# Optimization experiments

Hardware: AMD Instinct MI355X
Metric: run time of the kernel (lower is better)

Reference implementation:

```python
import math
import jax, jax.numpy as jnp
import numpy as np

T, B, F = 2048, 8, 768
N_HEAD = 12            # only used for the scale, per original code
N_CHUNK = 3            # chunk(3, -1) -> 3 effective heads
SCALE = math.sqrt(F // N_HEAD)  # sqrt(64) = 8.0


def setup_inputs() -> dict:
    key = jax.random.key(0)
    ks = jax.random.split(key, 9)
    s = 1.0 / math.sqrt(F)
    return {
        "x": jax.random.normal(ks[0], (T, B, F), jnp.float32),
        "Wq": jax.random.normal(ks[1], (F, F), jnp.float32) * s,
        "bq": jax.random.normal(ks[2], (F,), jnp.float32) * s,
        "Wk": jax.random.normal(ks[3], (F, F), jnp.float32) * s,
        "bk": jax.random.normal(ks[4], (F,), jnp.float32) * s,
        "Wv": jax.random.normal(ks[5], (F, F), jnp.float32) * s,
        "bv": jax.random.normal(ks[6], (F,), jnp.float32) * s,
        "Wo": jax.random.normal(ks[7], (F, F), jnp.float32) * s,
        "bo": jax.random.normal(ks[8], (F,), jnp.float32) * s,
    }


def reference(x, Wq, bq, Wk, bk, Wv, bv, Wo, bo):
    # x: (T, B, F). Linear is y = x @ W.T + b (torch convention).
    t, b, f = x.shape
    dh = f // N_CHUNK
    scale = jnp.asarray(SCALE, x.dtype)
    # project then split into 3 chunks along feature dim -> (T, B, 3, dh)
    q = (x @ Wq.T + bq).reshape(t, b, N_CHUNK, dh)
    k = (x @ Wk.T + bk).reshape(t, b, N_CHUNK, dh)
    v = (x @ Wv.T + bv).reshape(t, b, N_CHUNK, dh)
    # scores: (B, H, T, T)
    scores = jnp.einsum('tbhd,sbhd->bhts', q, k) / scale
    attn = jax.nn.softmax(scores, axis=-1)
    # output: (T, B, H, dh) -> (T, B, F)
    o = jnp.einsum('bhts,sbhd->tbhd', attn, v).reshape(t, b, f)
    return o @ Wo.T + bo
```

## Files before the change

kernel.cpp:

```cpp
#include <hip/hip_runtime.h>
#include <cstdint>
#include <cstddef>

#define T_SEQ 2048
#define B_SZ  8
#define F_DIM 768
#define H_CNT 3
#define DH    256

typedef float floatx4 __attribute__((ext_vector_type(4)));
typedef short bf16x8  __attribute__((ext_vector_type(8)));

static __device__ __forceinline__ unsigned short f2bf(float f) {
    union { float f; unsigned int i; } x; x.f = f;
    unsigned int r = (x.i + 0x7fffu + ((x.i >> 16) & 1u)) >> 16;
    return (unsigned short)r;
}

static __device__ __forceinline__ bf16x8 load8f(const float* __restrict__ p) {
    const floatx4 a = *(const floatx4*)p;
    const floatx4 b = *(const floatx4*)(p + 4);
    bf16x8 r;
#pragma unroll
    for (int i = 0; i < 4; ++i) r[i] = (short)f2bf(a[i]);
#pragma unroll
    for (int i = 0; i < 4; ++i) r[i + 4] = (short)f2bf(b[i]);
    return r;
}

#define ASYNC16(g, l) __builtin_amdgcn_global_load_lds( \
    (__attribute__((address_space(1))) void*)(void*)(g), \
    (__attribute__((address_space(3))) void*)(l), 16, 0, 0)

template<int AMODE, int CMODE>
__global__ __launch_bounds__(256, 2) void gemm_nt(
    const void* __restrict__ Av,
    const float* __restrict__ W,
    const float* __restrict__ bias,
    void* __restrict__ Cv,
    int M, int N, int K, float scale)
{
    __shared__ __align__(16) unsigned short As[128 * 32];
    __shared__ __align__(16) unsigned short Bs[128 * 32];

    const int tid  = threadIdx.x;
    const int wave = tid >> 6;
    const int lane = tid & 63;
    const int m0 = blockIdx.y * 128;
    const int n0 = blockIdx.x * 128;
    const int wm = (wave >> 1) * 64;
    const int wn = (wave & 1) * 64;
    const int q4 = lane >> 4;
    const int rr = lane & 15;

    const int lrow = lane >> 2;
    const int lk8  = (lane & 3) * 8;
    const int ar0 = wave * 16 + lrow;
    const int ar1 = (wave + 4) * 16 + lrow;

    floatx4 acc[4][4];
#pragma unroll
    for (int i = 0; i < 4; ++i)
#pragma unroll
        for (int j = 0; j < 4; ++j) acc[i][j] = (floatx4)0.0f;

    for (int k0 = 0; k0 < K; k0 += 32) {
        bf16x8 a0, a1;
        if (AMODE == 0) {
            const float* A = (const float*)Av;
            a0 = load8f(A + (size_t)(m0 + ar0) * K + k0 + lk8);
            a1 = load8f(A + (size_t)(m0 + ar1) * K + k0 + lk8);
        } else {
            const unsigned short* A = (const unsigned short*)Av;
            a0 = *(const bf16x8*)(A + (size_t)(m0 + ar0) * K + k0 + lk8);
            a1 = *(const bf16x8*)(A + (size_t)(m0 + ar1) * K + k0 + lk8);
        }
        bf16x8 b0 = load8f(W + (size_t)(n0 + ar0) * K + k0 + lk8);
        bf16x8 b1 = load8f(W + (size_t)(n0 + ar1) * K + k0 + lk8);
        __syncthreads();
        *(bf16x8*)&As[ar0 * 32 + lk8] = a0;
        *(bf16x8*)&As[ar1 * 32 + lk8] = a1;
        *(bf16x8*)&Bs[ar0 * 32 + lk8] = b0;
        *(bf16x8*)&Bs[ar1 * 32 + lk8] = b1;
        __syncthreads();

        bf16x8 af[4], bfv[4];
#pragma unroll
        for (int mt = 0; mt < 4; ++mt)
            af[mt] = *(const bf16x8*)&As[(wm + mt * 16 + rr) * 32 + q4 * 8];
#pragma unroll
        for (int nt = 0; nt < 4; ++nt)
            bfv[nt] = *(const bf16x8*)&Bs[(wn + nt * 16 + rr) * 32 + q4 * 8];
#pragma unroll
        for (int mt = 0; mt < 4; ++mt)
#pragma unroll
            for (int nt = 0; nt < 4; ++nt)
                acc[mt][nt] = __builtin_amdgcn_mfma_f32_16x16x32_bf16(af[mt], bfv[nt], acc[mt][nt], 0, 0, 0);
    }

#pragma unroll
    for (int nt = 0; nt < 4; ++nt) {
        const int col = n0 + wn + nt * 16 + rr;
        const float bv = bias[col];
#pragma unroll
        for (int mt = 0; mt < 4; ++mt) {
#pragma unroll
            for (int r = 0; r < 4; ++r) {
                const int row = m0 + wm + mt * 16 + q4 * 4 + r;
                const float v = (acc[mt][nt][r] + bv) * scale;
                if (CMODE == 2) {
                    ((float*)Cv)[(size_t)row * N + col] = v;
                } else {
                    const int t = row >> 3, bb = row & 7;
                    const int h = col >> 8, d = col & 255;
                    const size_t hb = (size_t)(bb * H_CNT + h) * (T_SEQ * DH);
                    size_t idx;
                    if (CMODE == 3) {
                        const int sblk = t >> 4, rrq = t & 15;
                        const int kc = d >> 5, q4v = (d >> 3) & 3, e = d & 7;
                        idx = hb + (size_t)(((sblk * 8 + kc) * 64 + q4v * 16 + rrq) * 8 + e);
                    } else {
                        const int skc = t >> 5, q4v = (t >> 3) & 3, e = t & 7;
                        const int dblk = d >> 4, rrq = d & 15;
                        idx = hb + (size_t)(((skc * 16 + dblk) * 64 + q4v * 16 + rrq) * 8 + e);
                    }
                    ((unsigned short*)Cv)[idx] = f2bf(v);
                }
            }
        }
    }
}

__global__ __launch_bounds__(256, 3) void attn_kernel(
    const unsigned short* __restrict__ Qf,
    const unsigned short* __restrict__ Kf,
    const unsigned short* __restrict__ Vf,
    unsigned short* __restrict__ Ob)
{
    __shared__ __align__(16) unsigned short Ks[8192];
    __shared__ __align__(16) unsigned short Vs[8192];
    __shared__ __align__(16) unsigned short Plds[4][512];

    const int tid  = threadIdx.x;
    const int wave = tid >> 6;
    const int lane = tid & 63;
    const int q4 = lane >> 4;
    const int rr = lane & 15;
    const int bh = blockIdx.y;
    const int b  = bh / H_CNT;
    const int h  = bh % H_CNT;
    const size_t hb = (size_t)bh * (T_SEQ * DH);

    const int qblk = blockIdx.x * 4 + wave;
    bf16x8 qf[8];
#pragma unroll
    for (int kc = 0; kc < 8; ++kc)
        qf[kc] = *(const bf16x8*)(Qf + hb + ((size_t)(qblk * 8 + kc) * 64 + lane) * 8);

    float m_[4], l_[4];
#pragma unroll
    for (int r = 0; r < 4; ++r) { m_[r] = -1e9f; l_[r] = 0.0f; }
    floatx4 oacc[16];
#pragma unroll
    for (int nt = 0; nt < 16; ++nt) oacc[nt] = (floatx4)0.0f;

    const int so = wave * 512 + lane * 8;

    for (int s0 = 0; s0 < T_SEQ; s0 += 32) {
        const unsigned short* kg = Kf + hb + (size_t)(s0 >> 4) * 4096;
        const unsigned short* vg = Vf + hb + (size_t)(s0 >> 5) * 8192;
#pragma unroll
        for (int rnd = 0; rnd < 4; ++rnd) {
            ASYNC16(kg + rnd * 2048 + so, (unsigned short*)Ks + rnd * 2048 + wave * 512);
            ASYNC16(vg + rnd * 2048 + so, (unsigned short*)Vs + rnd * 2048 + wave * 512);
        }
        __syncthreads();

        floatx4 sacc[2] = { (floatx4)0.0f, (floatx4)0.0f };
#pragma unroll
        for (int nt = 0; nt < 2; ++nt)
#pragma unroll
            for (int kc = 0; kc < 8; ++kc) {
                bf16x8 kf = *(const bf16x8*)&Ks[((nt * 8 + kc) * 64 + lane) * 8];
                sacc[nt] = __builtin_amdgcn_mfma_f32_16x16x32_bf16(qf[kc], kf, sacc[nt], 0, 0, 0);
            }

        float alpha[4];
#pragma unroll
        for (int r = 0; r < 4; ++r) {
            float s0v = sacc[0][r];
            float s1v = sacc[1][r];
            float cm = fmaxf(s0v, s1v);
            cm = fmaxf(cm, __shfl_xor(cm, 1));
            cm = fmaxf(cm, __shfl_xor(cm, 2));
            cm = fmaxf(cm, __shfl_xor(cm, 4));
            cm = fmaxf(cm, __shfl_xor(cm, 8));
            float mn = fmaxf(m_[r], cm);
            alpha[r] = __expf(m_[r] - mn);
            float p0 = __expf(s0v - mn);
            float p1 = __expf(s1v - mn);
            sacc[0][r] = p0; sacc[1][r] = p1;
            float rs = p0 + p1;
            rs += __shfl_xor(rs, 1);
            rs += __shfl_xor(rs, 2);
            rs += __shfl_xor(rs, 4);
            rs += __shfl_xor(rs, 8);
            l_[r] = alpha[r] * l_[r] + rs;
            m_[r] = mn;
        }

        unsigned short* pw = Plds[wave];
#pragma unroll
        for (int nt = 0; nt < 2; ++nt)
#pragma unroll
            for (int r = 0; r < 4; ++r)
                pw[(q4 * 4 + r) * 32 + nt * 16 + rr] = f2bf(sacc[nt][r]);
        bf16x8 pf = *(const bf16x8*)&pw[rr * 32 + q4 * 8];

#pragma unroll
        for (int nt = 0; nt < 16; ++nt) {
#pragma unroll
            for (int r = 0; r < 4; ++r) oacc[nt][r] *= alpha[r];
        }
#pragma unroll
        for (int nt = 0; nt < 16; ++nt) {
            bf16x8 vf = *(const bf16x8*)&Vs[(nt * 64 + lane) * 8];
            oacc[nt] = __builtin_amdgcn_mfma_f32_16x16x32_bf16(pf, vf, oacc[nt], 0, 0, 0);
        }
        __syncthreads();
    }

#pragma unroll
    for (int r = 0; r < 4; ++r) {
        const float inv_l = 1.0f / fmaxf(l_[r], 1e-30f);
        const int t = qblk * 16 + q4 * 4 + r;
#pragma unroll
        for (int nt = 0; nt < 16; ++nt) {
            const int col = h * DH + nt * 16 + rr;
            const float v = oacc[nt][r] * inv_l;
            Ob[((size_t)(t * B_SZ + b)) * F_DIM + col] = f2bf(v);
        }
    }
}

extern "C" void kernel_launch(void* const* d_in, const int* in_sizes, int n_in,
                              void* d_out, int out_size, void* d_ws, size_t ws_size,
                              hipStream_t stream)
{
    const float* x  = (const float*)d_in[0];
    const float* Wq = (const float*)d_in[1];
    const float* bq = (const float*)d_in[2];
    const float* Wk = (const float*)d_in[3];
    const float* bk = (const float*)d_in[4];
    const float* Wv = (const float*)d_in[5];
    const float* bv = (const float*)d_in[6];
    const float* Wo = (const float*)d_in[7];
    const float* bo = (const float*)d_in[8];
    float* out = (float*)d_out;

    const int M = T_SEQ * B_SZ;
    const int N = F_DIM, K = F_DIM;
    const size_t E = (size_t)M * F_DIM;

    unsigned short* Qf = (unsigned short*)d_ws;
    unsigned short* Kb = Qf + E;
    unsigned short* Vb = Kb + E;
    unsigned short* Ob = Vb + E;

    dim3 g(N / 128, M / 128), blk(256);
    gemm_nt<0, 3><<<g, blk, 0, stream>>>(x, Wq, bq, Qf, M, N, K, 0.125f);
    gemm_nt<0, 3><<<g, blk, 0, stream>>>(x, Wk, bk, Kb, M, N, K, 1.0f);
    gemm_nt<0, 4><<<g, blk, 0, stream>>>(x, Wv, bv, Vb, M, N, K, 1.0f);
    attn_kernel<<<dim3(T_SEQ / 64, B_SZ * H_CNT), blk, 0, stream>>>(Qf, Kb, Vb, Ob);
    gemm_nt<1, 2><<<g, blk, 0, stream>>>(Ob, Wo, bo, out, M, N, K, 1.0f);
}
```

Measured before the change: 562.5 us.

## Restructure attention to 2 waves with 32 query rows each and transposed MFMA

The attention kernel now runs 128-thread blocks in which each wave owns two 16-row query tiles. Each K and V fragment read from LDS is reused across both query tiles, and operands are swapped so the softmax row reductions need only two cross-lane shuffles. Output rescaling is skipped when no row maximum changed, and outputs are stored as packed pairs. In the GEMMs, bf16 conversion uses cheaper round-half-up packing via perm, and the bf16 A operand is loaded asynchronously straight into LDS. The costs are more registers per wave, fewer waves per block, and slightly different bf16 rounding.

```diff
diff --git a/kernel.cpp b/kernel.cpp
--- a/kernel.cpp
+++ b/kernel.cpp
@@ -13,19 +13,19 @@
 
 static __device__ __forceinline__ unsigned short f2bf(float f) {
     union { float f; unsigned int i; } x; x.f = f;
-    unsigned int r = (x.i + 0x7fffu + ((x.i >> 16) & 1u)) >> 16;
-    return (unsigned short)r;
-}
-
-static __device__ __forceinline__ bf16x8 load8f(const float* __restrict__ p) {
+    return (unsigned short)((x.i + 0x8000u) >> 16);
+}
+static __device__ __forceinline__ unsigned int pkbf(float a, float b) {
+    union { float f; unsigned int i; } xa, xb; xa.f = a; xb.f = b;
+    return __builtin_amdgcn_perm(xb.i + 0x8000u, xa.i + 0x8000u, 0x07060302u);
+}
+static __device__ __forceinline__ bf16x8 cvt8(const float* __restrict__ p) {
     const floatx4 a = *(const floatx4*)p;
     const floatx4 b = *(const floatx4*)(p + 4);
-    bf16x8 r;
-#pragma unroll
-    for (int i = 0; i < 4; ++i) r[i] = (short)f2bf(a[i]);
-#pragma unroll
-    for (int i = 0; i < 4; ++i) r[i + 4] = (short)f2bf(b[i]);
-    return r;
+    union { unsigned int u[4]; bf16x8 v; } r;
+    r.u[0] = pkbf(a[0], a[1]); r.u[1] = pkbf(a[2], a[3]);
+    r.u[2] = pkbf(b[0], b[1]); r.u[3] = pkbf(b[2], b[3]);
+    return r.v;
 }
 
 #define ASYNC16(g, l) __builtin_amdgcn_global_load_lds( \
@@ -68,18 +68,20 @@
         bf16x8 a0, a1;
         if (AMODE == 0) {
             const float* A = (const float*)Av;
-            a0 = load8f(A + (size_t)(m0 + ar0) * K + k0 + lk8);
-            a1 = load8f(A + (size_t)(m0 + ar1) * K + k0 + lk8);
+            a0 = cvt8(A + (size_t)(m0 + ar0) * K + k0 + lk8);
+            a1 = cvt8(A + (size_t)(m0 + ar1) * K + k0 + lk8);
+        }
+        bf16x8 b0 = cvt8(W + (size_t)(n0 + ar0) * K + k0 + lk8);
+        bf16x8 b1 = cvt8(W + (size_t)(n0 + ar1) * K + k0 + lk8);
+        __syncthreads();
+        if (AMODE == 0) {
+            *(bf16x8*)&As[ar0 * 32 + lk8] = a0;
+            *(bf16x8*)&As[ar1 * 32 + lk8] = a1;
         } else {
             const unsigned short* A = (const unsigned short*)Av;
-            a0 = *(const bf16x8*)(A + (size_t)(m0 + ar0) * K + k0 + lk8);
-            a1 = *(const bf16x8*)(A + (size_t)(m0 + ar1) * K + k0 + lk8);
-        }
-        bf16x8 b0 = load8f(W + (size_t)(n0 + ar0) * K + k0 + lk8);
-        bf16x8 b1 = load8f(W + (size_t)(n0 + ar1) * K + k0 + lk8);
-        __syncthreads();
-        *(bf16x8*)&As[ar0 * 32 + lk8] = a0;
-        *(bf16x8*)&As[ar1 * 32 + lk8] = a1;
+            ASYNC16(A + (size_t)(m0 + ar0) * K + k0 + lk8, (unsigned short*)As + wave * 512);
+            ASYNC16(A + (size_t)(m0 + ar1) * K + k0 + lk8, (unsigned short*)As + (wave + 4) * 512);
+        }
         *(bf16x8*)&Bs[ar0 * 32 + lk8] = b0;
         *(bf16x8*)&Bs[ar1 * 32 + lk8] = b1;
         __syncthreads();
@@ -131,7 +133,7 @@
     }
 }
 
-__global__ __launch_bounds__(256, 3) void attn_kernel(
+__global__ __launch_bounds__(128, 2) void attn_kernel(
     const unsigned short* __restrict__ Qf,
     const unsigned short* __restrict__ Kf,
     const unsigned short* __restrict__ Vf,
@@ -139,7 +141,7 @@
 {
     __shared__ __align__(16) unsigned short Ks[8192];
     __shared__ __align__(16) unsigned short Vs[8192];
-    __shared__ __align__(16) unsigned short Plds[4][512];
+    __shared__ __align__(16) unsigned short Ps[2][32 * 40];
 
     const int tid  = threadIdx.x;
     const int wave = tid >> 6;
@@ -151,94 +153,118 @@
     const int h  = bh % H_CNT;
     const size_t hb = (size_t)bh * (T_SEQ * DH);
 
-    const int qblk = blockIdx.x * 4 + wave;
-    bf16x8 qf[8];
-#pragma unroll
-    for (int kc = 0; kc < 8; ++kc)
-        qf[kc] = *(const bf16x8*)(Qf + hb + ((size_t)(qblk * 8 + kc) * 64 + lane) * 8);
-
-    float m_[4], l_[4];
-#pragma unroll
-    for (int r = 0; r < 4; ++r) { m_[r] = -1e9f; l_[r] = 0.0f; }
-    floatx4 oacc[16];
-#pragma unroll
-    for (int nt = 0; nt < 16; ++nt) oacc[nt] = (floatx4)0.0f;
-
-    const int so = wave * 512 + lane * 8;
+    const int sb0 = blockIdx.x * 4 + wave * 2;
+    bf16x8 qf_[2][8];
+#pragma unroll
+    for (int qnt = 0; qnt < 2; ++qnt)
+#pragma unroll
+        for (int kc = 0; kc < 8; ++kc)
+            qf_[qnt][kc] = *(const bf16x8*)(Qf + hb + ((size_t)((sb0 + qnt) * 8 + kc) * 64 + lane) * 8);
+
+    float m_[2] = { -1e9f, -1e9f }, l_[2] = { 0.0f, 0.0f };
+    floatx4 oacc[16][2];
+#pragma unroll
+    for (int dt = 0; dt < 16; ++dt)
+#pragma unroll
+        for (int qnt = 0; qnt < 2; ++qnt) oacc[dt][qnt] = (floatx4)0.0f;
+
+    const int sbase = wave * 4096 + lane * 8;
 
     for (int s0 = 0; s0 < T_SEQ; s0 += 32) {
         const unsigned short* kg = Kf + hb + (size_t)(s0 >> 4) * 4096;
         const unsigned short* vg = Vf + hb + (size_t)(s0 >> 5) * 8192;
 #pragma unroll
-        for (int rnd = 0; rnd < 4; ++rnd) {
-            ASYNC16(kg + rnd * 2048 + so, (unsigned short*)Ks + rnd * 2048 + wave * 512);
-            ASYNC16(vg + rnd * 2048 + so, (unsigned short*)Vs + rnd * 2048 + wave * 512);
+        for (int rnd = 0; rnd < 8; ++rnd) {
+            ASYNC16(kg + sbase + rnd * 512, (unsigned short*)Ks + wave * 4096 + rnd * 512);
+            ASYNC16(vg + sbase + rnd * 512, (unsigned short*)Vs + wave * 4096 + rnd * 512);
         }
         __syncthreads();
 
-        floatx4 sacc[2] = { (floatx4)0.0f, (floatx4)0.0f };
-#pragma unroll
-        for (int nt = 0; nt < 2; ++nt)
-#pragma unroll
-            for (int kc = 0; kc < 8; ++kc) {
-                bf16x8 kf = *(const bf16x8*)&Ks[((nt * 8 + kc) * 64 + lane) * 8];
-                sacc[nt] = __builtin_amdgcn_mfma_f32_16x16x32_bf16(qf[kc], kf, sacc[nt], 0, 0, 0);
-            }
-
-        float alpha[4];
-#pragma unroll
-        for (int r = 0; r < 4; ++r) {
-            float s0v = sacc[0][r];
-            float s1v = sacc[1][r];
-            float cm = fmaxf(s0v, s1v);
-            cm = fmaxf(cm, __shfl_xor(cm, 1));
-            cm = fmaxf(cm, __shfl_xor(cm, 2));
-            cm = fmaxf(cm, __shfl_xor(cm, 4));
-            cm = fmaxf(cm, __shfl_xor(cm, 8));
-            float mn = fmaxf(m_[r], cm);
-            alpha[r] = __expf(m_[r] - mn);
-            float p0 = __expf(s0v - mn);
-            float p1 = __expf(s1v - mn);
-            sacc[0][r] = p0; sacc[1][r] = p1;
-            float rs = p0 + p1;
-            rs += __shfl_xor(rs, 1);
-            rs += __shfl_xor(rs, 2);
-            rs += __shfl_xor(rs, 4);
-            rs += __shfl_xor(rs, 8);
-            l_[r] = alpha[r] * l_[r] + rs;
-            m_[r] = mn;
-        }
-
-        unsigned short* pw = Plds[wave];
-#pragma unroll
-        for (int nt = 0; nt < 2; ++nt)
-#pragma unroll
-            for (int r = 0; r < 4; ++r)
-                pw[(q4 * 4 + r) * 32 + nt * 16 + rr] = f2bf(sacc[nt][r]);
-        bf16x8 pf = *(const bf16x8*)&pw[rr * 32 + q4 * 8];
-
-#pragma unroll
-        for (int nt = 0; nt < 16; ++nt) {
-#pragma unroll
-            for (int r = 0; r < 4; ++r) oacc[nt][r] *= alpha[r];
-        }
-#pragma unroll
-        for (int nt = 0; nt < 16; ++nt) {
-            bf16x8 vf = *(const bf16x8*)&Vs[(nt * 64 + lane) * 8];
-            oacc[nt] = __builtin_amdgcn_mfma_f32_16x16x32_bf16(pf, vf, oacc[nt], 0, 0, 0);
+        floatx4 sacc[2][2];
+#pragma unroll
+        for (int i = 0; i < 2; ++i)
+#pragma unroll
+            for (int j = 0; j < 2; ++j) sacc[i][j] = (floatx4)0.0f;
+#pragma unroll
+        for (int kc = 0; kc < 8; ++kc) {
+            bf16x8 k0 = *(const bf16x8*)&Ks[((0 * 8 + kc) * 64 + lane) * 8];
+            bf16x8 k1 = *(const bf16x8*)&Ks[((1 * 8 + kc) * 64 + lane) * 8];
+            sacc[0][0] = __builtin_amdgcn_mfma_f32_16x16x32_bf16(k0, qf_[0][kc], sacc[0][0], 0, 0, 0);
+            sacc[0][1] = __builtin_amdgcn_mfma_f32_16x16x32_bf16(k0, qf_[1][kc], sacc[0][1], 0, 0, 0);
+            sacc[1][0] = __builtin_amdgcn_mfma_f32_16x16x32_bf16(k1, qf_[0][kc], sacc[1][0], 0, 0, 0);
+            sacc[1][1] = __builtin_amdgcn_mfma_f32_16x16x32_bf16(k1, qf_[1][kc], sacc[1][1], 0, 0, 0);
+        }
+
+        float alpha[2];
+        int upd = 0;
+#pragma unroll
+        for (int qnt = 0; qnt < 2; ++qnt) {
+            float cm = sacc[0][qnt][0];
+#pragma unroll
+            for (int smt = 0; smt < 2; ++smt)
+#pragma unroll
+                for (int r = 0; r < 4; ++r) cm = fmaxf(cm, sacc[smt][qnt][r]);
+            cm = fmaxf(cm, __shfl_xor(cm, 16));
+            cm = fmaxf(cm, __shfl_xor(cm, 32));
+            const float mn = fmaxf(m_[qnt], cm);
+            alpha[qnt] = __expf(m_[qnt] - mn);
+            float rs = 0.0f;
+#pragma unroll
+            for (int smt = 0; smt < 2; ++smt)
+#pragma unroll
+                for (int r = 0; r < 4; ++r) {
+                    const float p = __expf(sacc[smt][qnt][r] - mn);
+                    sacc[smt][qnt][r] = p; rs += p;
+                }
+            rs += __shfl_xor(rs, 16);
+            rs += __shfl_xor(rs, 32);
+            l_[qnt] = alpha[qnt] * l_[qnt] + rs;
+            upd |= (mn > m_[qnt]);
+            m_[qnt] = mn;
+        }
+
+        unsigned short* pw = Ps[wave];
+#pragma unroll
+        for (int qnt = 0; qnt < 2; ++qnt)
+#pragma unroll
+            for (int smt = 0; smt < 2; ++smt)
+#pragma unroll
+                for (int r = 0; r < 4; ++r)
+                    pw[(qnt * 16 + rr) * 40 + smt * 16 + q4 * 4 + r] = f2bf(sacc[smt][qnt][r]);
+        bf16x8 pf0 = *(const bf16x8*)&pw[(0 * 16 + rr) * 40 + q4 * 8];
+        bf16x8 pf1 = *(const bf16x8*)&pw[(1 * 16 + rr) * 40 + q4 * 8];
+
+        if (__any(upd)) {
+#pragma unroll
+            for (int dt = 0; dt < 16; ++dt)
+#pragma unroll
+                for (int qnt = 0; qnt < 2; ++qnt)
+#pragma unroll
+                    for (int r = 0; r < 4; ++r) oacc[dt][qnt][r] *= alpha[qnt];
+        }
+
+#pragma unroll
+        for (int dt = 0; dt < 16; ++dt) {
+            bf16x8 vf = *(const bf16x8*)&Vs[(dt * 64 + lane) * 8];
+            oacc[dt][0] = __builtin_amdgcn_mfma_f32_16x16x32_bf16(vf, pf0, oacc[dt][0], 0, 0, 0);
+            oacc[dt][1] = __builtin_amdgcn_mfma_f32_16x16x32_bf16(vf, pf1, oacc[dt][1], 0, 0, 0);
         }
         __syncthreads();
     }
 
 #pragma unroll
-    for (int r = 0; r < 4; ++r) {
-        const float inv_l = 1.0f / fmaxf(l_[r], 1e-30f);
-        const int t = qblk * 16 + q4 * 4 + r;
-#pragma unroll
-        for (int nt = 0; nt < 16; ++nt) {
-            const int col = h * DH + nt * 16 + rr;
-            const float v = oacc[nt][r] * inv_l;
-            Ob[((size_t)(t * B_SZ + b)) * F_DIM + col] = f2bf(v);
+    for (int qnt = 0; qnt < 2; ++qnt) {
+        const float inv_l = 1.0f / fmaxf(l_[qnt], 1e-30f);
+        const int t = blockIdx.x * 64 + wave * 32 + qnt * 16 + rr;
+        unsigned short* orow = Ob + (size_t)(t * B_SZ + b) * F_DIM + h * DH;
+#pragma unroll
+        for (int dt = 0; dt < 16; ++dt) {
+#pragma unroll
+            for (int rp = 0; rp < 2; ++rp) {
+                const unsigned int w = pkbf(oacc[dt][qnt][rp * 2] * inv_l,
+                                            oacc[dt][qnt][rp * 2 + 1] * inv_l);
+                *(unsigned int*)(orow + dt * 16 + q4 * 4 + rp * 2) = w;
+            }
         }
     }
 }
@@ -271,6 +297,6 @@
     gemm_nt<0, 3><<<g, blk, 0, stream>>>(x, Wq, bq, Qf, M, N, K, 0.125f);
     gemm_nt<0, 3><<<g, blk, 0, stream>>>(x, Wk, bk, Kb, M, N, K, 1.0f);
     gemm_nt<0, 4><<<g, blk, 0, stream>>>(x, Wv, bv, Vb, M, N, K, 1.0f);
-    attn_kernel<<<dim3(T_SEQ / 64, B_SZ * H_CNT), blk, 0, stream>>>(Qf, Kb, Vb, Ob);
+    attn_kernel<<<dim3(T_SEQ / 64, B_SZ * H_CNT), dim3(128), 0, stream>>>(Qf, Kb, Vb, Ob);
     gemm_nt<1, 2><<<g, blk, 0, stream>>>(Ob, Wo, bo, out, M, N, K, 1.0f);
 }
```

New measurement: 473.5 us. -15.8%, faster.
